# Performance work log

Measured on AMD Instinct MI355X. Metric: run time of the kernel, lower is better.

## Reference

```python
import jax, jax.numpy as jnp
import numpy as np
from jax import lax

A, B, L, FC, H, NR, NC, NF, K = 64, 256, 2000, 64, 128, 512, 10000, 1000000, 5


def setup_inputs() -> dict:
    key = jax.random.key(0)
    ks = jax.random.split(key, 16)
    s = 0.1
    return {
        "bincounts": jax.random.uniform(ks[0], (B, L), jnp.float32) * 10.0,
        "conv1_w": jax.random.normal(ks[1], (FC // 2, 1, K), jnp.float32) * s,
        "conv1_b": jax.random.normal(ks[2], (FC // 2,), jnp.float32) * s,
        "conv2_w": jax.random.normal(ks[3], (FC, FC // 2, K), jnp.float32) * s,
        "conv2_b": jax.random.normal(ks[4], (FC,), jnp.float32) * s,
        "lin1_w": jax.random.normal(ks[5], (H, FC), jnp.float32) * s,
        "lin1_b": jax.random.normal(ks[6], (H,), jnp.float32) * s,
        "lin2_w": jax.random.normal(ks[7], (H, H), jnp.float32) * s,
        "lin2_b": jax.random.normal(ks[8], (H,), jnp.float32) * s,
        "baseline_table": jax.random.normal(ks[9], (NR, L), jnp.float32) * s,
        "differential": jax.random.normal(ks[10], (A, H), jnp.float32) * s,
        "regions_oi": jax.random.randint(ks[11], (B,), 0, NR, jnp.int32),
        "labels": jax.random.randint(ks[12], (NC,), 0, A, jnp.int32),
        "local_cell_ix": jax.random.randint(ks[13], (NF,), 0, NC, jnp.int32),
        "local_region_ix": jax.random.randint(ks[14], (NF,), 0, B, jnp.int32),
        "binixs": jax.random.randint(ks[15], (NF, 1), 0, L, jnp.int32),
    }


def _conv1d_same(x, w, b):
    # x: (B, Cin, L), w: (Cout, Cin, K) -> (B, Cout, L)
    y = lax.conv_general_dilated(x, w, (1,), "SAME",
                                 dimension_numbers=("NCH", "OIH", "NCH"))
    return y + b[None, :, None]


def reference(bincounts, conv1_w, conv1_b, conv2_w, conv2_b,
              lin1_w, lin1_b, lin2_w, lin2_b,
              baseline_table, differential,
              regions_oi, labels, local_cell_ix, local_region_ix, binixs):
    # conv backbone: (B, 1, L) -> (B, FC, L)
    x = bincounts[:, None, :]
    h = _conv1d_same(x, conv1_w, conv1_b)
    h = _conv1d_same(h, conv2_w, conv2_b)
    # MLP per (region, bin): (B, L, FC) -> (B, L, H)
    e = h.transpose(0, 2, 1)
    e = jax.nn.relu(e @ lin1_w.T + lin1_b)
    e = jax.nn.relu(e @ lin2_w.T + lin2_b)
    # baseline per selected region: (B, L)
    base = baseline_table[regions_oi]
    # einsum 'bcd,ad->abc': (A, B, L)
    u = jnp.einsum("bld,ad->abl", e, differential) + base[None]
    heights = jax.nn.log_softmax(u, axis=-1) + jnp.float32(np.log(u.shape[1]))
    # multi-index gather over fragments
    return heights[labels[local_cell_ix], local_region_ix, binixs[:, 0]]
```

## Files before the change

kernel.cpp:

```cpp
#include <hip/hip_runtime.h>
#include <stdint.h>

typedef unsigned int u32;
typedef short v8s __attribute__((ext_vector_type(8)));
typedef float v4f __attribute__((ext_vector_type(4)));

#define B_ 256
#define NF_ 1000000
#define LN_A 5.545177444479562f

__device__ inline u32 f2bf1(float a) {
    u32 x = __float_as_uint(a);
    return (x + 0x7fffu + ((x >> 16) & 1u)) >> 16;
}
__device__ inline float bfval(float a) { return __uint_as_float(f2bf1(a) << 16); }
__device__ inline u32 packbf(float lo, float hi) { return f2bf1(lo) | (f2bf1(hi) << 16); }
__device__ inline v8s as_v8s(uint4 x) { union { uint4 a; v8s b; } u; u.a = x; return u.b; }
__device__ inline v4f mfma16(v8s a, v8s b, v4f c) {
    return __builtin_amdgcn_mfma_f32_16x16x32_bf16(a, b, c, 0, 0, 0);
}
__device__ inline void wave_lds_fence() {
    asm volatile("s_waitcnt lgkmcnt(0)" ::: "memory");
}

__device__ inline void split8(const float* p, v8s& hi, v8s& lo) {
    u32 h[4], l[4];
    #pragma unroll
    for (int i = 0; i < 4; ++i) {
        float2 f = *(const float2*)(p + 2*i);
        u32 xa = __float_as_uint(f.x), xb = __float_as_uint(f.y);
        h[i] = __builtin_amdgcn_perm(xb, xa, 0x07060302u);
        float la = f.x - __uint_as_float(xa & 0xffff0000u);
        float lb = f.y - __uint_as_float(xb & 0xffff0000u);
        l[i] = __builtin_amdgcn_perm(__float_as_uint(lb), __float_as_uint(la), 0x07060302u);
    }
    hi = as_v8s(make_uint4(h[0], h[1], h[2], h[3]));
    lo = as_v8s(make_uint4(l[0], l[1], l[2], l[3]));
}

#define OFF_W2T_H 8192
#define OFF_W2T_L 16384
#define OFF_DIFF_H 24576
#define OFF_DIFF_L 28672
#define OFF_WCOMP 32768
#define OFF_BCOMP 33344
#define OFF_VC    33408
#define OFF_CW    102400
#define OFF_CB1   103680
#define OFF_PART  131072
#define OFF_VC1   655360

__global__ __launch_bounds__(256) void w_prep(
    const float* __restrict__ x,   const float* __restrict__ w1c,
    const float* __restrict__ b1c, const float* __restrict__ w2c,
    const float* __restrict__ b2c, const float* __restrict__ w2l,
    const float* __restrict__ diff, u32* __restrict__ scr)
{
    int idx = blockIdx.x * 256 + threadIdx.x;
    float* scf = (float*)scr;
    if (idx < 8192) {
        int inew = idx >> 2, comp = idx & 3;
        int nt = inew >> 8, kc = (inew >> 6) & 3, lane = inew & 63;
        int j = nt*16 + (lane & 15);
        int c = kc*16 + (lane >> 4)*4 + comp;
        float v0 = w2l[j*128 + 2*c], v1 = w2l[j*128 + 2*c + 1];
        scr[OFF_W2T_H + idx] = packbf(v0, v1);
        scr[OFF_W2T_L + idx] = packbf(v0 - bfval(v0), v1 - bfval(v1));
    } else if (idx < 12288) {
        int r = idx - 8192;
        int inew = r >> 2, comp = r & 3;
        int nt = inew >> 8, kc = (inew >> 6) & 3, lane = inew & 63;
        int a = nt*16 + (lane & 15);
        int c = kc*16 + (lane >> 4)*4 + comp;
        float v0 = diff[a*128 + 2*c], v1 = diff[a*128 + 2*c + 1];
        scr[OFF_DIFF_H + r] = packbf(v0, v1);
        scr[OFF_DIFF_L + r] = packbf(v0 - bfval(v0), v1 - bfval(v1));
    } else if (idx < 12864) {
        int r = idx - 12288, j = r >> 6, o = r & 63;
        float s = 0.0f;
        for (int k1 = 0; k1 < 5; ++k1) {
            int k2 = j - k1;
            if (k2 < 0 || k2 > 4) continue;
            for (int i = 0; i < 32; ++i)
                s += w1c[i*5 + k1] * w2c[o*160 + i*5 + k2];
        }
        scf[OFF_WCOMP + r] = s;
    } else if (idx < 12928) {
        int o = idx - 12864;
        float s = b2c[o];
        for (int i = 0; i < 32; ++i) {
            float b1 = b1c[i];
            for (int k2 = 0; k2 < 5; ++k2) s += w2c[o*160 + i*5 + k2] * b1;
        }
        scf[OFF_BCOMP + o] = s;
    } else if (idx >= 13056 && idx < 78592) {
        int r = idx - 13056;
        int b = r >> 8, q = (r >> 6) & 3, o = r & 63;
        float x0 = x[b*2000], x1 = x[b*2000 + 1];
        float xa = x[b*2000 + 1998], xb = x[b*2000 + 1999];
        float s = 0.0f;
        for (int i = 0; i < 32; ++i) {
            float b1 = b1c[i];
            if (q == 0) {
                float hvm2 = b1 + w1c[i*5 + 4]*x0;
                float hvm1 = b1 + w1c[i*5 + 3]*x0 + w1c[i*5 + 4]*x1;
                s += w2c[o*160 + i*5 + 0]*hvm2 + w2c[o*160 + i*5 + 1]*hvm1;
            } else if (q == 1) {
                float hvm1 = b1 + w1c[i*5 + 3]*x0 + w1c[i*5 + 4]*x1;
                s += w2c[o*160 + i*5 + 0]*hvm1;
            } else if (q == 2) {
                float hv0 = b1 + w1c[i*5 + 0]*xa + w1c[i*5 + 1]*xb;
                s += w2c[o*160 + i*5 + 4]*hv0;
            } else {
                float hv0 = b1 + w1c[i*5 + 0]*xa + w1c[i*5 + 1]*xb;
                float hv1 = b1 + w1c[i*5 + 0]*xb;
                s += w2c[o*160 + i*5 + 3]*hv0 + w2c[o*160 + i*5 + 4]*hv1;
            }
        }
        scf[OFF_VC + r] = s;
    }
}

__global__ __launch_bounds__(256) void k_prep2(
    const float* __restrict__ w1l, const float* __restrict__ b1l,
    u32* __restrict__ scr)
{
    __shared__ float w1s[8192];
    for (int i = threadIdx.x; i < 8192; i += 256) w1s[i] = w1l[i];
    __syncthreads();

    const float* scf = (const float*)scr;
    float* out = (float*)scr;
    int idx = blockIdx.x * 256 + threadIdx.x;
    if (idx < 1152) {
        int tap = idx >> 7, j = idx & 127;
        float s = 0.f;
        for (int o = 0; o < 64; ++o)
            s += w1s[j*64 + o] * scf[OFF_WCOMP + tap*64 + o];
        out[OFF_CW + idx] = s;
    } else if (idx < 1280) {
        int j = idx - 1152;
        float s = b1l[j];
        for (int o = 0; o < 64; ++o)
            s += w1s[j*64 + o] * scf[OFF_BCOMP + o];
        out[OFF_CB1 + j] = s;
    } else if (idx < 1280 + 131072) {
        int r = idx - 1280;
        int bq = r >> 7, j = r & 127;
        float s = 0.f;
        for (int o = 0; o < 64; ++o)
            s += w1s[j*64 + o] * scf[OFF_VC + bq*64 + o];
        out[OFF_VC1 + r] = s;
    }
}

__global__ __launch_bounds__(256, 3) void k_front(
    const float* __restrict__ x,   const float* __restrict__ b2l,
    const float* __restrict__ CW,  const float* __restrict__ cb1,
    const float* __restrict__ Vc1,
    const uint4* __restrict__ w2h, const uint4* __restrict__ w2lo,
    const uint4* __restrict__ dh,  const uint4* __restrict__ dl,
    const float* __restrict__ baseline, const int* __restrict__ regions,
    float* __restrict__ U, float* __restrict__ partials)
{
    __shared__ float smf[9136];
    const int b     = blockIdx.x >> 4;
    const int chunk = blockIdx.x & 15;
    const int t     = threadIdx.x;
    const int lane  = t & 63;
    const int w     = __builtin_amdgcn_readfirstlane(t >> 6);
    const int n16   = lane & 15;
    const int q     = lane >> 4;
    const int l0w   = (chunk << 7) + w*32;
    const int rrow  = regions[b];

    float* Aw   = smf + w*2156;
    float* xsw  = Aw + 2112;
    float* sred = smf + 8624;
    u32*  estd  = (u32*)Aw;
    uint16_t* esth = (uint16_t*)Aw;

    if (lane < 44) {
        int g = l0w - 4 + lane;
        xsw[lane] = (g >= 0 && g < 2000) ? x[b*2000 + g] : 0.0f;
    }
    wave_lds_fence();

    float cw0[9], cw1[9];
    #pragma unroll
    for (int d = 0; d < 9; ++d) {
        float2 c2 = *(const float2*)&CW[d*128 + 2*lane];
        cw0[d] = c2.x; cw1[d] = c2.y;
    }
    const float2 cb2 = *(const float2*)&cb1[2*lane];

    float blv[2][4];
    bool  vl[2][4];
    #pragma unroll
    for (int mt = 0; mt < 2; ++mt)
        #pragma unroll
        for (int rg = 0; rg < 4; ++rg) {
            int rl = l0w + mt*16 + q*4 + rg;
            vl[mt][rg] = rl < 2000;
            blv[mt][rg] = baseline[rrow*2000 + (rl < 2000 ? rl : 1999)];
        }

    v8s a2h[2][4], a2l[2][4];
    #pragma unroll
    for (int mt = 0; mt < 2; ++mt) {
        float win[9];
        #pragma unroll
        for (int d = 0; d < 9; ++d) win[d] = xsw[mt*16 + d];
        #pragma unroll
        for (int r = 0; r < 16; ++r) {
            int gl = l0w + mt*16 + r;
            float h0 = cb2.x, h1v = cb2.y;
            #pragma unroll
            for (int d = 0; d < 9; ++d) { h0 += win[d]*cw0[d]; h1v += win[d]*cw1[d]; }
            if (gl <= 1) {
                float2 v = *(const float2*)&Vc1[(b*4 + gl)*128 + 2*lane];
                h0 -= v.x; h1v -= v.y;
            } else if (gl >= 1998 && gl < 2000) {
                float2 v = *(const float2*)&Vc1[(b*4 + gl - 1996)*128 + 2*lane];
                h0 -= v.x; h1v -= v.y;
            }
            *(float2*)&Aw[r*130 + 2*lane] = make_float2(fmaxf(h0, 0.f), fmaxf(h1v, 0.f));
            #pragma unroll
            for (int d = 0; d < 8; ++d) win[d] = win[d+1];
            win[8] = xsw[mt*16 + r + 9];
        }
        wave_lds_fence();
        #pragma unroll
        for (int kc = 0; kc < 4; ++kc)
            split8(&Aw[n16*130 + kc*32 + q*8], a2h[mt][kc], a2l[mt][kc]);
        wave_lds_fence();
    }

    v4f acc2[2][8];
    #pragma unroll
    for (int nt = 0; nt < 8; ++nt) {
        float bias = b2l[nt*16 + n16];
        acc2[0][nt] = (v4f){bias, bias, bias, bias};
        acc2[1][nt] = (v4f){bias, bias, bias, bias};
    }
    #pragma unroll
    for (int nt = 0; nt < 8; ++nt) {
        #pragma unroll
        for (int kc = 0; kc < 4; ++kc) {
            v8s bh = as_v8s(w2h [(nt*4 + kc)*64 + lane]);
            v8s bl = as_v8s(w2lo[(nt*4 + kc)*64 + lane]);
            acc2[0][nt] = mfma16(a2h[0][kc], bh, acc2[0][nt]);
            acc2[0][nt] = mfma16(a2l[0][kc], bh, acc2[0][nt]);
            acc2[0][nt] = mfma16(a2h[0][kc], bl, acc2[0][nt]);
            acc2[1][nt] = mfma16(a2h[1][kc], bh, acc2[1][nt]);
            acc2[1][nt] = mfma16(a2l[1][kc], bh, acc2[1][nt]);
            acc2[1][nt] = mfma16(a2h[1][kc], bl, acc2[1][nt]);
        }
    }

    #pragma unroll
    for (int mt = 0; mt < 2; ++mt)
        #pragma unroll
        for (int nt = 0; nt < 8; ++nt)
            #pragma unroll
            for (int rg = 0; rg < 4; ++rg) {
                float v = fmaxf(acc2[mt][nt][rg], 0.0f);
                int rr = mt*16 + q*4 + rg;
                esth[rr*132 + nt*16 + n16] = (uint16_t)f2bf1(v);
            }
    wave_lds_fence();

    v8s af[2][4];
    #pragma unroll
    for (int mt = 0; mt < 2; ++mt)
        #pragma unroll
        for (int kc = 0; kc < 4; ++kc) {
            int ba = (mt*16 + n16)*66 + kc*16 + q*4;
            uint2 p0 = *(const uint2*)(estd + ba);
            uint2 p1 = *(const uint2*)(estd + ba + 2);
            af[mt][kc] = as_v8s(make_uint4(p0.x, p0.y, p1.x, p1.y));
        }
    wave_lds_fence();

    #pragma unroll
    for (int nt = 0; nt < 4; ++nt) {
        v4f acc0 = (v4f){0.f,0.f,0.f,0.f}, acc1 = (v4f){0.f,0.f,0.f,0.f};
        #pragma unroll
        for (int kc = 0; kc < 4; ++kc) {
            v8s bh = as_v8s(dh[(nt*4 + kc)*64 + lane]);
            v8s bl = as_v8s(dl[(nt*4 + kc)*64 + lane]);
            acc0 = mfma16(af[0][kc], bh, acc0);
            acc1 = mfma16(af[1][kc], bh, acc1);
            acc0 = mfma16(af[0][kc], bl, acc0);
            acc1 = mfma16(af[1][kc], bl, acc1);
        }
        #pragma unroll
        for (int rg = 0; rg < 4; ++rg) {
            Aw[(q*4 + rg)*65      + nt*16 + n16] = acc0[rg] + blv[0][rg];
            Aw[(16 + q*4 + rg)*65 + nt*16 + n16] = acc1[rg] + blv[1][rg];
        }
        float m = -3.0e38f, s = 0.0f;
        #pragma unroll
        for (int rg = 0; rg < 4; ++rg) {
            float u = acc0[rg] + blv[0][rg];
            if (vl[0][rg]) {
                float mn = fmaxf(m, u);
                s = s * __expf(m - mn) + __expf(u - mn);
                m = mn;
            }
        }
        #pragma unroll
        for (int rg = 0; rg < 4; ++rg) {
            float u = acc1[rg] + blv[1][rg];
            if (vl[1][rg]) {
                float mn = fmaxf(m, u);
                s = s * __expf(m - mn) + __expf(u - mn);
                m = mn;
            }
        }
        #pragma unroll
        for (int off = 16; off < 64; off <<= 1) {
            float m2 = __shfl_xor(m, off, 64);
            float s2 = __shfl_xor(s, off, 64);
            float mn = fmaxf(m, m2);
            s = s * __expf(m - mn) + s2 * __expf(m2 - mn);
            m = mn;
        }
        if (q == 0) {
            sred[(w*64 + nt*16 + n16)*2 + 0] = m;
            sred[(w*64 + nt*16 + n16)*2 + 1] = s;
        }
    }
    wave_lds_fence();

    #pragma unroll
    for (int c = 0; c < 8; ++c) {
        int row = c*4 + (lane >> 4);
        int col = (lane & 15) * 4;
        int glr = l0w + row;
        if (glr < 2000) {
            const float* src = Aw + row*65 + col;
            v4f v = {src[0], src[1], src[2], src[3]};
            __builtin_nontemporal_store(v, (v4f*)(U + ((size_t)(b*2000 + glr))*64 + col));
        }
    }

    __syncthreads();
    if (t < 64) {
        float m = sred[t*2 + 0], s = sred[t*2 + 1];
        #pragma unroll
        for (int ww = 1; ww < 4; ++ww) {
            float m2 = sred[(ww*64 + t)*2 + 0], s2 = sred[(ww*64 + t)*2 + 1];
            float mn = fmaxf(m, m2);
            s = s * __expf(m - mn) + s2 * __expf(m2 - mn);
            m = mn;
        }
        partials[((b*16 + chunk)*64 + t)*2 + 0] = m;
        partials[((b*16 + chunk)*64 + t)*2 + 1] = s;
    }
}

__global__ __launch_bounds__(64) void k_red(
    const float* __restrict__ partials, float* __restrict__ lse)
{
    int b = blockIdx.x, a = threadIdx.x;
    float m = -3.0e38f, s = 0.0f;
    for (int c = 0; c < 16; ++c) {
        float pm = partials[((b*16 + c)*64 + a)*2 + 0];
        float ps = partials[((b*16 + c)*64 + a)*2 + 1];
        float mn = fmaxf(m, pm);
        s = s * __expf(m - mn) + ps * __expf(pm - mn);
        m = mn;
    }
    lse[b*64 + a] = m + __logf(s);
}

__global__ __launch_bounds__(256) void k_gather2(
    const float* __restrict__ U, const float* __restrict__ lse,
    const int* __restrict__ labels, const int* __restrict__ cellix,
    const int* __restrict__ regionix, const int* __restrict__ binix,
    float* __restrict__ out)
{
    int f = blockIdx.x * 256 + threadIdx.x;
    if (f >= NF_) return;
    int b = regionix[f];
    int l = binix[f];
    int a = labels[cellix[f]];
    out[f] = U[((size_t)(b*2000 + l))*64 + a] - lse[b*64 + a] + LN_A;
}

extern "C" void kernel_launch(void* const* d_in, const int* in_sizes, int n_in,
                              void* d_out, int out_size, void* d_ws, size_t ws_size,
                              hipStream_t stream)
{
    const float* bincounts = (const float*)d_in[0];
    const float* conv1_w   = (const float*)d_in[1];
    const float* conv1_b   = (const float*)d_in[2];
    const float* conv2_w   = (const float*)d_in[3];
    const float* conv2_b   = (const float*)d_in[4];
    const float* lin1_w    = (const float*)d_in[5];
    const float* lin1_b    = (const float*)d_in[6];
    const float* lin2_w    = (const float*)d_in[7];
    const float* lin2_b    = (const float*)d_in[8];
    const float* baseline  = (const float*)d_in[9];
    const float* diff      = (const float*)d_in[10];
    const int*   regions   = (const int*)d_in[11];
    const int*   labels    = (const int*)d_in[12];
    const int*   cellix    = (const int*)d_in[13];
    const int*   regionix  = (const int*)d_in[14];
    const int*   binix     = (const int*)d_in[15];
    float* out = (float*)d_out;
    u32*   scr = (u32*)d_out;

    const size_t u_words = (size_t)B_ * 2000 * 64;
    const size_t need = u_words*4 + (size_t)B_*64*4;
    if (ws_size < need) return;
    float* U   = (float*)d_ws;
    float* lse = U + u_words;

    const float* scf = (const float*)scr;
    float* partials = (float*)(scr + OFF_PART);

    w_prep  <<<dim3(307), dim3(256), 0, stream>>>(bincounts, conv1_w, conv1_b, conv2_w,
                                                  conv2_b, lin2_w, diff, scr);
    k_prep2 <<<dim3(518), dim3(256), 0, stream>>>(lin1_w, lin1_b, scr);
    k_front <<<dim3(B_*16), dim3(256), 0, stream>>>(bincounts, lin2_b,
                                                    scf + OFF_CW, scf + OFF_CB1,
                                                    scf + OFF_VC1,
                                                    (const uint4*)(scr + OFF_W2T_H),
                                                    (const uint4*)(scr + OFF_W2T_L),
                                                    (const uint4*)(scr + OFF_DIFF_H),
                                                    (const uint4*)(scr + OFF_DIFF_L),
                                                    baseline, regions, U, partials);
    k_red   <<<dim3(B_), dim3(64), 0, stream>>>(partials, lse);
    k_gather2<<<dim3((NF_+255)/256), dim3(256), 0, stream>>>(U, lse, labels, cellix,
                                                             regionix, binix, out);
}
```

Before: 253.9 us.

## Cut register pressure in k_front to raise occupancy to four blocks per CU

Raises launch bounds from 3 to 4 blocks per CU and reduces live registers to make that fit. The second GEMM now runs in pairs of N-tiles with a small accumulator set instead of holding all 16 accumulators at once. The baseline loads move later so they are not live across the GEMMs. The online softmax reduction is replaced by a two-pass max-then-sum over 8 values with fewer exps. The added occupancy may bring spills, and the baseline loads now sit closer to their use and get less time to hide latency.

```diff
diff --git a/kernel.cpp b/kernel.cpp
--- a/kernel.cpp
+++ b/kernel.cpp
@@ -154,7 +154,7 @@
     }
 }
 
-__global__ __launch_bounds__(256, 3) void k_front(
+__global__ __launch_bounds__(256, 4) void k_front(
     const float* __restrict__ x,   const float* __restrict__ b2l,
     const float* __restrict__ CW,  const float* __restrict__ cb1,
     const float* __restrict__ Vc1,
@@ -193,17 +193,6 @@
         cw0[d] = c2.x; cw1[d] = c2.y;
     }
     const float2 cb2 = *(const float2*)&cb1[2*lane];
-
-    float blv[2][4];
-    bool  vl[2][4];
-    #pragma unroll
-    for (int mt = 0; mt < 2; ++mt)
-        #pragma unroll
-        for (int rg = 0; rg < 4; ++rg) {
-            int rl = l0w + mt*16 + q*4 + rg;
-            vl[mt][rg] = rl < 2000;
-            blv[mt][rg] = baseline[rrow*2000 + (rl < 2000 ? rl : 1999)];
-        }
 
     v8s a2h[2][4], a2l[2][4];
     #pragma unroll
@@ -236,38 +225,43 @@
         wave_lds_fence();
     }
 
-    v4f acc2[2][8];
-    #pragma unroll
-    for (int nt = 0; nt < 8; ++nt) {
-        float bias = b2l[nt*16 + n16];
-        acc2[0][nt] = (v4f){bias, bias, bias, bias};
-        acc2[1][nt] = (v4f){bias, bias, bias, bias};
-    }
-    #pragma unroll
-    for (int nt = 0; nt < 8; ++nt) {
-        #pragma unroll
-        for (int kc = 0; kc < 4; ++kc) {
-            v8s bh = as_v8s(w2h [(nt*4 + kc)*64 + lane]);
-            v8s bl = as_v8s(w2lo[(nt*4 + kc)*64 + lane]);
-            acc2[0][nt] = mfma16(a2h[0][kc], bh, acc2[0][nt]);
-            acc2[0][nt] = mfma16(a2l[0][kc], bh, acc2[0][nt]);
-            acc2[0][nt] = mfma16(a2h[0][kc], bl, acc2[0][nt]);
-            acc2[1][nt] = mfma16(a2h[1][kc], bh, acc2[1][nt]);
-            acc2[1][nt] = mfma16(a2l[1][kc], bh, acc2[1][nt]);
-            acc2[1][nt] = mfma16(a2h[1][kc], bl, acc2[1][nt]);
-        }
-    }
-
-    #pragma unroll
-    for (int mt = 0; mt < 2; ++mt)
-        #pragma unroll
-        for (int nt = 0; nt < 8; ++nt)
+    #pragma unroll
+    for (int np = 0; np < 4; ++np) {
+        v4f acc[2][2];
+        #pragma unroll
+        for (int i = 0; i < 2; ++i) {
+            float bias = b2l[(np*2 + i)*16 + n16];
+            acc[0][i] = (v4f){bias, bias, bias, bias};
+            acc[1][i] = (v4f){bias, bias, bias, bias};
+        }
+        #pragma unroll
+        for (int i = 0; i < 2; ++i) {
+            int nt = np*2 + i;
             #pragma unroll
-            for (int rg = 0; rg < 4; ++rg) {
-                float v = fmaxf(acc2[mt][nt][rg], 0.0f);
-                int rr = mt*16 + q*4 + rg;
-                esth[rr*132 + nt*16 + n16] = (uint16_t)f2bf1(v);
+            for (int kc = 0; kc < 4; ++kc) {
+                v8s bh = as_v8s(w2h [(nt*4 + kc)*64 + lane]);
+                v8s bl = as_v8s(w2lo[(nt*4 + kc)*64 + lane]);
+                acc[0][i] = mfma16(a2h[0][kc], bh, acc[0][i]);
+                acc[0][i] = mfma16(a2l[0][kc], bh, acc[0][i]);
+                acc[0][i] = mfma16(a2h[0][kc], bl, acc[0][i]);
+                acc[1][i] = mfma16(a2h[1][kc], bh, acc[1][i]);
+                acc[1][i] = mfma16(a2l[1][kc], bh, acc[1][i]);
+                acc[1][i] = mfma16(a2h[1][kc], bl, acc[1][i]);
             }
+        }
+        #pragma unroll
+        for (int i = 0; i < 2; ++i) {
+            int nt = np*2 + i;
+            #pragma unroll
+            for (int mt = 0; mt < 2; ++mt)
+                #pragma unroll
+                for (int rg = 0; rg < 4; ++rg) {
+                    float v = fmaxf(acc[mt][i][rg], 0.0f);
+                    int rr = mt*16 + q*4 + rg;
+                    esth[rr*132 + nt*16 + n16] = (uint16_t)f2bf1(v);
+                }
+        }
+    }
     wave_lds_fence();
 
     v8s af[2][4];
@@ -281,6 +275,17 @@
             af[mt][kc] = as_v8s(make_uint4(p0.x, p0.y, p1.x, p1.y));
         }
     wave_lds_fence();
+
+    float blv[2][4];
+    bool  vl[2][4];
+    #pragma unroll
+    for (int mt = 0; mt < 2; ++mt)
+        #pragma unroll
+        for (int rg = 0; rg < 4; ++rg) {
+            int rl = l0w + mt*16 + q*4 + rg;
+            vl[mt][rg] = rl < 2000;
+            blv[mt][rg] = baseline[rrow*2000 + (rl < 2000 ? rl : 1999)];
+        }
 
     #pragma unroll
     for (int nt = 0; nt < 4; ++nt) {
@@ -294,40 +299,28 @@
             acc0 = mfma16(af[0][kc], bl, acc0);
             acc1 = mfma16(af[1][kc], bl, acc1);
         }
+        float uu[8];
         #pragma unroll
         for (int rg = 0; rg < 4; ++rg) {
-            Aw[(q*4 + rg)*65      + nt*16 + n16] = acc0[rg] + blv[0][rg];
-            Aw[(16 + q*4 + rg)*65 + nt*16 + n16] = acc1[rg] + blv[1][rg];
-        }
-        float m = -3.0e38f, s = 0.0f;
-        #pragma unroll
-        for (int rg = 0; rg < 4; ++rg) {
-            float u = acc0[rg] + blv[0][rg];
-            if (vl[0][rg]) {
-                float mn = fmaxf(m, u);
-                s = s * __expf(m - mn) + __expf(u - mn);
-                m = mn;
-            }
-        }
-        #pragma unroll
-        for (int rg = 0; rg < 4; ++rg) {
-            float u = acc1[rg] + blv[1][rg];
-            if (vl[1][rg]) {
-                float mn = fmaxf(m, u);
-                s = s * __expf(m - mn) + __expf(u - mn);
-                m = mn;
-            }
-        }
-        #pragma unroll
-        for (int off = 16; off < 64; off <<= 1) {
-            float m2 = __shfl_xor(m, off, 64);
-            float s2 = __shfl_xor(s, off, 64);
-            float mn = fmaxf(m, m2);
-            s = s * __expf(m - mn) + s2 * __expf(m2 - mn);
-            m = mn;
-        }
+            float u0 = acc0[rg] + blv[0][rg];
+            float u1 = acc1[rg] + blv[1][rg];
+            Aw[(q*4 + rg)*65      + nt*16 + n16] = u0;
+            Aw[(16 + q*4 + rg)*65 + nt*16 + n16] = u1;
+            uu[rg]     = vl[0][rg] ? u0 : -3.0e38f;
+            uu[4 + rg] = vl[1][rg] ? u1 : -3.0e38f;
+        }
+        float M = uu[0];
+        #pragma unroll
+        for (int j = 1; j < 8; ++j) M = fmaxf(M, uu[j]);
+        M = fmaxf(M, __shfl_xor(M, 16, 64));
+        M = fmaxf(M, __shfl_xor(M, 32, 64));
+        float s = 0.0f;
+        #pragma unroll
+        for (int j = 0; j < 8; ++j) s += __expf(uu[j] - M);
+        s += __shfl_xor(s, 16, 64);
+        s += __shfl_xor(s, 32, 64);
         if (q == 0) {
-            sred[(w*64 + nt*16 + n16)*2 + 0] = m;
+            sred[(w*64 + nt*16 + n16)*2 + 0] = M;
             sred[(w*64 + nt*16 + n16)*2 + 1] = s;
         }
     }
```

New measurement: 228.6 us. 1.11x faster.
